# Kernel optimization log

Hardware: AMD Instinct MI355X
Metric: run time of the kernel (lower is better)

Reference implementation:

```python
import jax, jax.numpy as jnp
import numpy as np

B, T, I, H, O = 128, 2048, 128, 256, 128


def _lstm_step(h, c, x_t, wx, bx, wh, bh):
    # gates: [B, 4H], chunk order: input, forget, cell, output
    gates = x_t @ wx.T + bx + h @ wh.T + bh
    i_g, f_g, g_g, o_g = jnp.split(gates, 4, axis=1)
    i_t = jax.nn.sigmoid(i_g)
    f_t = jax.nn.sigmoid(f_g)
    g_t = jnp.tanh(g_g)
    o_t = jax.nn.sigmoid(o_g)
    cy = c * f_t + i_t * g_t
    hy = o_t * jnp.tanh(cy)
    return hy, cy


def _gru_step(h, x_t, wx, bx, wh, bh):
    # chunk order: reset, update, new
    x_g = x_t @ wx.T + bx
    h_g = h @ wh.T + bh
    x_r, x_z, x_n = jnp.split(x_g, 3, axis=1)
    h_r, h_z, h_n = jnp.split(h_g, 3, axis=1)
    r = jax.nn.sigmoid(x_r + h_r)
    z = jax.nn.sigmoid(x_z + h_z)
    n = jnp.tanh(x_n + r * h_n)
    return z * h + (1.0 - z) * n


def _run_direction(x_tbi, w1x, b1x, w1h, b1h, w2x, b2x, w2h, b2h):
    # x_tbi: [T, B, I]; returns final hidden of top cell [B, H]
    h1 = jnp.zeros((x_tbi.shape[1], H), x_tbi.dtype)
    c1 = jnp.zeros_like(h1)
    h2 = jnp.zeros_like(h1)

    def step(carry, x_t):
        h1, c1, h2 = carry
        h1, c1 = _lstm_step(h1, c1, x_t, w1x, b1x, w1h, b1h)
        h2 = _gru_step(h2, h1, w2x, b2x, w2h, b2h)
        return (h1, c1, h2), None

    (h1, c1, h2), _ = jax.lax.scan(step, (h1, c1, h2), x_tbi)
    return h2


def setup_inputs() -> dict:
    key = jax.random.key(0)
    ks = jax.random.split(key, 8)
    std1 = 1.0 / np.sqrt(H)
    u = lambda k, shape, s: jax.random.uniform(k, shape, jnp.float32, -s, s)
    x = jax.random.normal(ks[0], (B, T, I), jnp.float32)
    # Cell 1: LSTM(input=I, hidden=H)
    w1x = u(ks[1], (4 * H, I), std1)
    b1x = jnp.zeros((4 * H,), jnp.float32)
    w1h = u(ks[2], (4 * H, H), std1)
    b1h = jnp.zeros((4 * H,), jnp.float32)
    # Cell 2: GRU(input=H, hidden=H)
    w2x = u(ks[3], (3 * H, H), std1)
    b2x = jnp.zeros((3 * H,), jnp.float32)
    w2h = u(ks[4], (3 * H, H), std1)
    b2h = jnp.zeros((3 * H,), jnp.float32)
    # out_fc: Linear(2H -> O), kaiming-normal fan_in
    wo = jax.random.normal(ks[5], (O, 2 * H), jnp.float32) * np.sqrt(2.0 / (2 * H))
    bo = jnp.zeros((O,), jnp.float32)
    return {"x": x, "w1x": w1x, "b1x": b1x, "w1h": w1h, "b1h": b1h,
            "w2x": w2x, "b2x": b2x, "w2h": w2h, "b2h": b2h, "wo": wo, "bo": bo}


def reference(x, w1x, b1x, w1h, b1h, w2x, b2x, w2h, b2h, wo, bo):
    x_tbi = jnp.swapaxes(x, 0, 1)  # [T, B, I]
    h_fwd = _run_direction(x_tbi, w1x, b1x, w1h, b1h, w2x, b2x, w2h, b2h)
    h_bwd = _run_direction(x_tbi[::-1], w1x, b1x, w1h, b1h, w2x, b2x, w2h, b2h)
    h_cat = jnp.concatenate([h_fwd, h_bwd], axis=1)  # [B, 2H]
    return h_cat @ wo.T + bo  # [B, O]
```

## Files before the change

### kernel.cpp

```cpp
#include <hip/hip_runtime.h>

#define T_LEN 2048
#define I_DIM 128
#define H_DIM 256


#define XHI_OFF 0
#define XLO_OFF 8192
#define CRED_OFF 16384
#define LDS_BYTES 98304

typedef __attribute__((ext_vector_type(8))) short short8;
typedef __attribute__((ext_vector_type(16))) float f32x16;

__device__ __forceinline__ float sigmoidf_(float v) { return 1.f / (1.f + __expf(-v)); }
__device__ __forceinline__ float tanhf_fast(float v) {
    float t = __expf(-2.f * fabsf(v));
    float r = (1.f - t) / (1.f + t);
    return v < 0.f ? -r : r;
}
__device__ __forceinline__ unsigned short bf16_rne(float f) {
    unsigned u = __float_as_uint(f);
    return (unsigned short)((u + 0x7fffu + ((u >> 16) & 1u)) >> 16);
}
__device__ __forceinline__ void split2(float a, unsigned short& h, unsigned short& l) {
    h = bf16_rne(a);
    float hf = __uint_as_float(((unsigned)h) << 16);
    l = bf16_rne(a - hf);
}
__device__ __forceinline__ short8 ld_frag(const char* p) {
    union { unsigned long long u[2]; short8 s; } v;
    v.u[0] = __hip_atomic_load((const unsigned long long*)p,
                               __ATOMIC_RELAXED, __HIP_MEMORY_SCOPE_AGENT);
    v.u[1] = __hip_atomic_load((const unsigned long long*)(p + 8),
                               __ATOMIC_RELAXED, __HIP_MEMORY_SCOPE_AGENT);
    return v.s;
}

__device__ __forceinline__ void stage_unit(const float* __restrict__ x, char* smem_b,
                                           int b0, int teff, int b, int cq) {
    const float4* src = (const float4*)(x + ((size_t)(b0 + b) * T_LEN + teff) * I_DIM + cq * 16);
    float4 v0 = src[0], v1 = src[1], v2 = src[2], v3 = src[3];
    float f[16] = {v0.x, v0.y, v0.z, v0.w, v1.x, v1.y, v1.z, v1.w,
                   v2.x, v2.y, v2.z, v2.w, v3.x, v3.y, v3.z, v3.w};
    short8 H0, H1, L0, L1;
    #pragma unroll
    for (int e = 0; e < 8; ++e) {
        unsigned short h, l;
        split2(f[e], h, l);      H0[e] = (short)h; L0[e] = (short)l;
        split2(f[8 + e], h, l);  H1[e] = (short)h; L1[e] = (short)l;
    }
    char* bh = smem_b + XHI_OFF + cq * 1024 + b * 16;
    char* bl = smem_b + XLO_OFF + cq * 1024 + b * 16;
    *(short8*)bh = H0; *(short8*)(bh + 512) = H1;
    *(short8*)bl = L0; *(short8*)(bl + 512) = L1;
}

#define MFMA3(ac, ah, al, bh, bl)                                              \
    ac = __builtin_amdgcn_mfma_f32_32x32x16_bf16(ah, bh, ac, 0, 0, 0);         \
    ac = __builtin_amdgcn_mfma_f32_32x32x16_bf16(ah, bl, ac, 0, 0, 0);         \
    ac = __builtin_amdgcn_mfma_f32_32x32x16_bf16(al, bh, ac, 0, 0, 0);

#define ACCSEL(i) ((i & 3) == 0 ? acc0 : (i & 3) == 1 ? acc1 : (i & 3) == 2 ? acc2 : acc3)

__global__ __launch_bounds__(256, 1)
void brnn_persistent(const float* __restrict__ x,
                     const float* __restrict__ w1x, const float* __restrict__ b1x,
                     const float* __restrict__ w1h, const float* __restrict__ b1h,
                     const float* __restrict__ w2x, const float* __restrict__ b2x,
                     const float* __restrict__ w2h, const float* __restrict__ b2h,
                     int* flags, char* exgb, float* h2out)
{
    extern __shared__ char smem_b[];

    const int tid  = threadIdx.x;
    const int lane = tid & 63;
    const int wid  = tid >> 6;
    const int wg   = blockIdx.x;
    const int grp  = wg & 7;
    const int cu   = wg >> 3;
    const int dir  = grp >> 2;
    const int btile = grp & 3;
    const int b0   = btile * 32;

    int* flg = flags + grp * 64;
    float* cred = (float*)(smem_b + CRED_OFF);

    const int nrow = lane & 31;
    const int jrow = nrow >> 2;
    const int q    = nrow & 3;
    const int half = lane >> 5;

    short8 BH[16], BL[16];
    #pragma unroll
    for (int i = 0; i < 16; ++i) {
        short8 H, L;
        #pragma unroll
        for (int e = 0; e < 8; ++e) {
            int kk = (i & 7) * 16 + half * 8 + e;
            float v = 0.f;
            if (wid == 0) {
                if (i < 8) {
                    int R = q * H_DIM + cu * 8 + jrow;
                    v = w1x[R * I_DIM + kk];
                }
            } else if (wid == 1) {
                int R = q * H_DIM + cu * 8 + jrow;
                if (i < 8) v = w1h[R * H_DIM + kk];
                else if (q < 3) v = w2x[(q * H_DIM + cu * 8 + jrow) * H_DIM + kk];
            } else if (wid == 2) {
                int R = q * H_DIM + cu * 8 + jrow;
                if (i < 8) v = w1h[R * H_DIM + 128 + kk];
                else if (q < 3) v = w2x[(q * H_DIM + cu * 8 + jrow) * H_DIM + 128 + kk];
            } else {
                int kk16 = i * 16 + half * 8 + e;
                if (q == 0)      v = w2h[(0 * H_DIM + cu * 8 + jrow) * H_DIM + kk16];
                else if (q == 1) v = w2h[(1 * H_DIM + cu * 8 + jrow) * H_DIM + kk16];
                else if (q == 3) v = w2h[(2 * H_DIM + cu * 8 + jrow) * H_DIM + kk16];
            }
            unsigned short hh, ll;
            split2(v, hh, ll);
            H[e] = (short)hh; L[e] = (short)ll;
        }
        BH[i] = H; BL[i] = L;
    }

    const int tt  = tid & 127;
    const int bbn = tt & 31;
    const int qn  = tt >> 5;
    float biasA[2][4];
    #pragma unroll
    for (int e = 0; e < 2; ++e) {
        int jg = cu * 8 + 2 * qn + e;
        if (tid < 128) {
            #pragma unroll
            for (int g = 0; g < 4; ++g)
                biasA[e][g] = b1x[g * H_DIM + jg] + b1h[g * H_DIM + jg];
        } else {
            biasA[e][0] = b2x[0 * H_DIM + jg] + b2h[0 * H_DIM + jg];
            biasA[e][1] = b2x[1 * H_DIM + jg] + b2h[1 * H_DIM + jg];
            biasA[e][2] = b2x[2 * H_DIM + jg];
            biasA[e][3] = b2h[2 * H_DIM + jg];
        }
    }
    float st[2] = {0.f, 0.f};

    if (tid < 128) {
        char* p1 = exgb + (size_t)(8 + grp) * 65536 + (tid >> 6) * 32768
                 + (cu >> 1) * 1024 + (cu & 1) * 512 + (tid & 63) * 8;
        __hip_atomic_store((unsigned long long*)p1, 0ull,
                           __ATOMIC_RELAXED, __HIP_MEMORY_SCOPE_AGENT);
    }
    stage_unit(x, smem_b, b0, dir ? (T_LEN - 1) : 0, tid >> 3, tid & 7);
    __syncthreads();
    if (tid == 0)
        __hip_atomic_store(&flg[cu], 4, __ATOMIC_RELAXED, __HIP_MEMORY_SCOPE_AGENT);

    for (int s = 0; s <= T_LEN; ++s) {
        {
            int tgt = 4 * (s + 1);
            const int* fp = &flg[lane & 31];
            while (true) {
                int v = (lane < 32)
                    ? __hip_atomic_load(fp, __ATOMIC_RELAXED, __HIP_MEMORY_SCOPE_AGENT)
                    : 0x7fffffff;
                if (__all(v >= tgt)) break;
            }
        }
        const char* exR = exgb + (size_t)(((s + 1) & 1) * 8 + grp) * 65536;
        char*       exW = exgb + (size_t)(((s)     & 1) * 8 + grp) * 65536;

        f32x16 acc0, acc1, acc2, acc3;
        #pragma unroll
        for (int r = 0; r < 16; ++r) { acc0[r]=0.f; acc1[r]=0.f; acc2[r]=0.f; acc3[r]=0.f; }

        if (wid == 0) {
            if (s < T_LEN) {
                #pragma unroll
                for (int i = 0; i < 8; ++i) {
                    short8 ah = *(const short8*)(smem_b + XHI_OFF + i * 1024 + lane * 16);
                    short8 al = *(const short8*)(smem_b + XLO_OFF + i * 1024 + lane * 16);
                    f32x16& ac = ACCSEL(i);
                    MFMA3(ac, ah, al, BH[i], BL[i]);
                }
                float* c0 = cred;
                #pragma unroll
                for (int r = 0; r < 16; ++r) {
                    int b = (r & 3) + 8 * (r >> 2) + 4 * half;
                    c0[nrow * 33 + b] = acc0[r] + acc1[r] + acc2[r] + acc3[r];
                }
            }
        } else if (wid < 3) {
            const int sb = (wid == 1) ? 0 : 8;
            short8 hA[8], lA[8];
            #pragma unroll
            for (int i = 0; i < 8; ++i) {
                hA[i] = ld_frag(exR + (sb + i) * 1024 + lane * 16);
                lA[i] = ld_frag(exR + 32768 + (sb + i) * 1024 + lane * 16);
            }
            if (s < T_LEN) {
                #pragma unroll
                for (int i = 0; i < 8; ++i) {
                    f32x16& ac = (i & 1) ? acc1 : acc0;
                    MFMA3(ac, hA[i], lA[i], BH[i], BL[i]);
                }
            }
            if (s >= 1) {
                #pragma unroll
                for (int i = 0; i < 8; ++i) {
                    f32x16& ac = (i & 1) ? acc3 : acc2;
                    MFMA3(ac, hA[i], lA[i], BH[8 + i], BL[8 + i]);
                }
            }
            float* cL = cred + wid * 1056;
            float* cX = cred + (2 + wid) * 1056;
            #pragma unroll
            for (int r = 0; r < 16; ++r) {
                int b = (r & 3) + 8 * (r >> 2) + 4 * half;
                cL[nrow * 33 + b] = acc0[r] + acc1[r];
                cX[nrow * 33 + b] = acc2[r] + acc3[r];
            }
        } else {
            if (s >= 1) {
                short8 hA[16], lA[16];
                #pragma unroll
                for (int i = 0; i < 16; ++i) {
                    hA[i] = ld_frag(exR + (16 + i) * 1024 + lane * 16);
                    lA[i] = ld_frag(exR + 32768 + (16 + i) * 1024 + lane * 16);
                }
                #pragma unroll
                for (int i = 0; i < 16; ++i) {
                    f32x16& ac = ACCSEL(i);
                    MFMA3(ac, hA[i], lA[i], BH[i], BL[i]);
                }
                float* c5 = cred + 5 * 1056;
                #pragma unroll
                for (int r = 0; r < 16; ++r) {
                    int b = (r & 3) + 8 * (r >> 2) + 4 * half;
                    c5[nrow * 33 + b] = acc0[r] + acc1[r] + acc2[r] + acc3[r];
                }
            }
        }
        __syncthreads();

        if (tid < 128) {
            if (s < T_LEN) {
                unsigned hi32 = 0, lo32 = 0;
                #pragma unroll
                for (int e = 0; e < 2; ++e) {
                    int j = 2 * qn + e;
                    float gi = cred[(j*4+0)*33+bbn] + cred[1056+(j*4+0)*33+bbn] + cred[2112+(j*4+0)*33+bbn] + biasA[e][0];
                    float gf = cred[(j*4+1)*33+bbn] + cred[1056+(j*4+1)*33+bbn] + cred[2112+(j*4+1)*33+bbn] + biasA[e][1];
                    float gg = cred[(j*4+2)*33+bbn] + cred[1056+(j*4+2)*33+bbn] + cred[2112+(j*4+2)*33+bbn] + biasA[e][2];
                    float go = cred[(j*4+3)*33+bbn] + cred[1056+(j*4+3)*33+bbn] + cred[2112+(j*4+3)*33+bbn] + biasA[e][3];
                    float ig = sigmoidf_(gi), fg = sigmoidf_(gf);
                    float cg = tanhf_fast(gg), og = sigmoidf_(go);
                    st[e] = st[e] * fg + ig * cg;
                    float h1v = og * tanhf_fast(st[e]);
                    unsigned short h, l;
                    split2(h1v, h, l);
                    hi32 |= ((unsigned)h) << (16 * e);
                    lo32 |= ((unsigned)l) << (16 * e);
                }
                int off = (cu >> 1) * 1024 + (cu & 1) * 512 + bbn * 16 + qn * 4;
                __hip_atomic_store((unsigned*)(exW + off), hi32,
                                   __ATOMIC_RELAXED, __HIP_MEMORY_SCOPE_AGENT);
                __hip_atomic_store((unsigned*)(exW + 32768 + off), lo32,
                                   __ATOMIC_RELAXED, __HIP_MEMORY_SCOPE_AGENT);
            }
        } else {
            if (s >= 1) {
                #pragma unroll
                for (int e = 0; e < 2; ++e) {
                    int j = 2 * qn + e;
                    float rc = cred[3*1056+(j*4+0)*33+bbn] + cred[4*1056+(j*4+0)*33+bbn]
                             + cred[5*1056+(j*4+0)*33+bbn] + biasA[e][0];
                    float zc = cred[3*1056+(j*4+1)*33+bbn] + cred[4*1056+(j*4+1)*33+bbn]
                             + cred[5*1056+(j*4+1)*33+bbn] + biasA[e][1];
                    float xn = cred[3*1056+(j*4+2)*33+bbn] + cred[4*1056+(j*4+2)*33+bbn] + biasA[e][2];
                    float hn = cred[5*1056+(j*4+3)*33+bbn] + biasA[e][3];
                    float rg = sigmoidf_(rc), zg = sigmoidf_(zc);
                    float ng = tanhf_fast(xn + rg * hn);
                    st[e] = zg * st[e] + (1.f - zg) * ng;
                }
            }
            if (s == T_LEN) {
                #pragma unroll
                for (int e = 0; e < 2; ++e)
                    h2out[(size_t)(grp * 32 + bbn) * H_DIM + cu * 8 + 2 * qn + e] = st[e];
            } else {
                unsigned hi32 = 0, lo32 = 0;
                #pragma unroll
                for (int e = 0; e < 2; ++e) {
                    unsigned short h, l;
                    split2(st[e], h, l);
                    hi32 |= ((unsigned)h) << (16 * e);
                    lo32 |= ((unsigned)l) << (16 * e);
                }
                int off = 16384 + (cu >> 1) * 1024 + (cu & 1) * 512 + bbn * 16 + qn * 4;
                __hip_atomic_store((unsigned*)(exW + off), hi32,
                                   __ATOMIC_RELAXED, __HIP_MEMORY_SCOPE_AGENT);
                __hip_atomic_store((unsigned*)(exW + 32768 + off), lo32,
                                   __ATOMIC_RELAXED, __HIP_MEMORY_SCOPE_AGENT);
            }
        }

        if (s == T_LEN) break;

        asm volatile("s_waitcnt vmcnt(0)" ::: "memory");
        if (lane == 0)
            __hip_atomic_fetch_add(&flg[cu], 1, __ATOMIC_RELAXED, __HIP_MEMORY_SCOPE_AGENT);
        if (wid == 0 && s + 1 < T_LEN) {
            int teff = dir ? (T_LEN - 2 - s) : (s + 1);
            #pragma unroll
            for (int i = 0; i < 4; ++i) {
                int u = i * 64 + lane;
                stage_unit(x, smem_b, b0, teff, u >> 3, u & 7);
            }
        }
    }
}

__global__ __launch_bounds__(128)
void brnn_out(const float* __restrict__ h2out, const float* __restrict__ wo,
              const float* __restrict__ bo, float* __restrict__ out)
{
    __shared__ float hc[512];
    int b = blockIdx.x;
    int o = threadIdx.x;
    int btile = b >> 5, bi = b & 31;
    for (int k = threadIdx.x; k < 256; k += 128) {
        hc[k]       = h2out[((size_t)(btile)     * 32 + bi) * H_DIM + k];
        hc[256 + k] = h2out[((size_t)(4 + btile) * 32 + bi) * H_DIM + k];
    }
    __syncthreads();
    float acc = bo[o];
    const float4* w4 = (const float4*)&wo[(size_t)o * 512];
    #pragma unroll 8
    for (int k = 0; k < 128; ++k) {
        float4 w = w4[k];
        acc += w.x * hc[k * 4] + w.y * hc[k * 4 + 1] + w.z * hc[k * 4 + 2] + w.w * hc[k * 4 + 3];
    }
    out[b * 128 + o] = acc;
}

extern "C" void kernel_launch(void* const* d_in, const int* in_sizes, int n_in,
                              void* d_out, int out_size, void* d_ws, size_t ws_size,
                              hipStream_t stream) {
    const float* x   = (const float*)d_in[0];
    const float* w1x = (const float*)d_in[1];
    const float* b1x = (const float*)d_in[2];
    const float* w1h = (const float*)d_in[3];
    const float* b1h = (const float*)d_in[4];
    const float* w2x = (const float*)d_in[5];
    const float* b2x = (const float*)d_in[6];
    const float* w2h = (const float*)d_in[7];
    const float* b2h = (const float*)d_in[8];
    const float* wo  = (const float*)d_in[9];
    const float* bo  = (const float*)d_in[10];
    float* out = (float*)d_out;

    char* ws = (char*)d_ws;
    int* flags = (int*)ws;
    char* exgb = ws + 4096;
    float* h2out = (float*)(ws + 4096 + 1048576);

    hipMemsetAsync(flags, 0, 8 * 64 * sizeof(int), stream);

    size_t shmem = LDS_BYTES;
    hipFuncSetAttribute((const void*)brnn_persistent,
                        hipFuncAttributeMaxDynamicSharedMemorySize, (int)shmem);

    void* args[] = { (void*)&x, (void*)&w1x, (void*)&b1x, (void*)&w1h, (void*)&b1h,
                     (void*)&w2x, (void*)&b2x, (void*)&w2h, (void*)&b2h,
                     (void*)&flags, (void*)&exgb, (void*)&h2out };
    hipError_t err = hipLaunchCooperativeKernel((void*)brnn_persistent,
                                                dim3(256), dim3(256), args,
                                                (unsigned int)shmem, stream);
    if (err != hipSuccess) {
        brnn_persistent<<<dim3(256), dim3(256), shmem, stream>>>(
            x, w1x, b1x, w1h, b1h, w2x, b2x, w2h, b2h, flags, exgb, h2out);
    }

    brnn_out<<<dim3(128), dim3(128), 0, stream>>>(h2out, wo, bo, out);
}
```

Before: 13.76 ms.

## Interleave forward and backward directions within each workgroup, halving grid size

Each workgroup now processes both the forward and backward direction for one batch tile, alternating phases so one direction's flag wait can overlap the other's compute. The grid shrinks from 256 to 128 workgroups, and LDS holds separate x staging buffers and reduction scratch for each direction. Per-step synchronisation changes from per-wave atomic increments to a block-wide __syncthreads followed by a single store of the step counter. The intent is to hide the cross-workgroup sync latency of the serial recurrence behind the other direction's work. The cost is twice the serial work per workgroup and an added block barrier on every phase.

```diff
diff --git a/kernel.cpp b/kernel.cpp
--- a/kernel.cpp
+++ b/kernel.cpp
@@ -5,9 +5,9 @@
 #define H_DIM 256
 
 
-#define XHI_OFF 0
-#define XLO_OFF 8192
-#define CRED_OFF 16384
+#define XA_OFF 0
+#define XB_OFF 16384
+#define CRED_OFF 32768
 #define LDS_BYTES 98304
 
 typedef __attribute__((ext_vector_type(8))) short short8;
@@ -37,7 +37,7 @@
     return v.s;
 }
 
-__device__ __forceinline__ void stage_unit(const float* __restrict__ x, char* smem_b,
+__device__ __forceinline__ void stage_unit(const float* __restrict__ x, char* xbuf,
                                            int b0, int teff, int b, int cq) {
     const float4* src = (const float4*)(x + ((size_t)(b0 + b) * T_LEN + teff) * I_DIM + cq * 16);
     float4 v0 = src[0], v1 = src[1], v2 = src[2], v3 = src[3];
@@ -50,8 +50,8 @@
         split2(f[e], h, l);      H0[e] = (short)h; L0[e] = (short)l;
         split2(f[8 + e], h, l);  H1[e] = (short)h; L1[e] = (short)l;
     }
-    char* bh = smem_b + XHI_OFF + cq * 1024 + b * 16;
-    char* bl = smem_b + XLO_OFF + cq * 1024 + b * 16;
+    char* bh = xbuf + cq * 1024 + b * 16;
+    char* bl = xbuf + 8192 + cq * 1024 + b * 16;
     *(short8*)bh = H0; *(short8*)(bh + 512) = H1;
     *(short8*)bl = L0; *(short8*)(bl + 512) = L1;
 }
@@ -77,14 +77,18 @@
     const int lane = tid & 63;
     const int wid  = tid >> 6;
     const int wg   = blockIdx.x;
-    const int grp  = wg & 7;
-    const int cu   = wg >> 3;
-    const int dir  = grp >> 2;
-    const int btile = grp & 3;
+    const int btile = wg & 3;
+    const int cu   = wg >> 2;
+    const int grpA = btile;
+    const int grpB = 4 + btile;
     const int b0   = btile * 32;
 
-    int* flg = flags + grp * 64;
-    float* cred = (float*)(smem_b + CRED_OFF);
+    int* flgA = flags + grpA * 64;
+    int* flgB = flags + grpB * 64;
+    float* credA = (float*)(smem_b + CRED_OFF);
+    float* credB = credA + 6 * 1056;
+    char* xbufA = smem_b + XA_OFF;
+    char* xbufB = smem_b + XB_OFF;
 
     const int nrow = lane & 31;
     const int jrow = nrow >> 2;
@@ -143,22 +147,31 @@
             biasA[e][3] = b2h[2 * H_DIM + jg];
         }
     }
-    float st[2] = {0.f, 0.f};
-
-    if (tid < 128) {
-        char* p1 = exgb + (size_t)(8 + grp) * 65536 + (tid >> 6) * 32768
+    float stA[2] = {0.f, 0.f};
+    float stB[2] = {0.f, 0.f};
+
+    {
+        int plane = (tid & 127) >> 6;
+        int g = (tid < 128) ? grpA : grpB;
+        char* p1 = exgb + (size_t)(8 + g) * 65536 + plane * 32768
                  + (cu >> 1) * 1024 + (cu & 1) * 512 + (tid & 63) * 8;
         __hip_atomic_store((unsigned long long*)p1, 0ull,
                            __ATOMIC_RELAXED, __HIP_MEMORY_SCOPE_AGENT);
     }
-    stage_unit(x, smem_b, b0, dir ? (T_LEN - 1) : 0, tid >> 3, tid & 7);
+    stage_unit(x, xbufA, b0, 0, tid >> 3, tid & 7);
+    stage_unit(x, xbufB, b0, T_LEN - 1, tid >> 3, tid & 7);
     __syncthreads();
-    if (tid == 0)
-        __hip_atomic_store(&flg[cu], 4, __ATOMIC_RELAXED, __HIP_MEMORY_SCOPE_AGENT);
-
-    for (int s = 0; s <= T_LEN; ++s) {
+    if (tid == 0) {
+        __hip_atomic_store(&flgA[cu], 1, __ATOMIC_RELAXED, __HIP_MEMORY_SCOPE_AGENT);
+        __hip_atomic_store(&flgB[cu], 1, __ATOMIC_RELAXED, __HIP_MEMORY_SCOPE_AGENT);
+    }
+
+    auto phase = [&](int grp, int dir, char* xbuf, float* cred6, int* flg,
+                     float (&st2)[2], int s) {
+        const char* exR = exgb + (size_t)(((s + 1) & 1) * 8 + grp) * 65536;
+        char*       exW = exgb + (size_t)(((s)     & 1) * 8 + grp) * 65536;
         {
-            int tgt = 4 * (s + 1);
+            int tgt = s + 1;
             const int* fp = &flg[lane & 31];
             while (true) {
                 int v = (lane < 32)
@@ -167,9 +180,6 @@
                 if (__all(v >= tgt)) break;
             }
         }
-        const char* exR = exgb + (size_t)(((s + 1) & 1) * 8 + grp) * 65536;
-        char*       exW = exgb + (size_t)(((s)     & 1) * 8 + grp) * 65536;
-
         f32x16 acc0, acc1, acc2, acc3;
         #pragma unroll
         for (int r = 0; r < 16; ++r) { acc0[r]=0.f; acc1[r]=0.f; acc2[r]=0.f; acc3[r]=0.f; }
@@ -178,12 +188,12 @@
             if (s < T_LEN) {
                 #pragma unroll
                 for (int i = 0; i < 8; ++i) {
-                    short8 ah = *(const short8*)(smem_b + XHI_OFF + i * 1024 + lane * 16);
-                    short8 al = *(const short8*)(smem_b + XLO_OFF + i * 1024 + lane * 16);
+                    short8 ah = *(const short8*)(xbuf + i * 1024 + lane * 16);
+                    short8 al = *(const short8*)(xbuf + 8192 + i * 1024 + lane * 16);
                     f32x16& ac = ACCSEL(i);
                     MFMA3(ac, ah, al, BH[i], BL[i]);
                 }
-                float* c0 = cred;
+                float* c0 = cred6;
                 #pragma unroll
                 for (int r = 0; r < 16; ++r) {
                     int b = (r & 3) + 8 * (r >> 2) + 4 * half;
@@ -212,8 +222,8 @@
                     MFMA3(ac, hA[i], lA[i], BH[8 + i], BL[8 + i]);
                 }
             }
-            float* cL = cred + wid * 1056;
-            float* cX = cred + (2 + wid) * 1056;
+            float* cL = cred6 + wid * 1056;
+            float* cX = cred6 + (2 + wid) * 1056;
             #pragma unroll
             for (int r = 0; r < 16; ++r) {
                 int b = (r & 3) + 8 * (r >> 2) + 4 * half;
@@ -233,7 +243,7 @@
                     f32x16& ac = ACCSEL(i);
                     MFMA3(ac, hA[i], lA[i], BH[i], BL[i]);
                 }
-                float* c5 = cred + 5 * 1056;
+                float* c5 = cred6 + 5 * 1056;
                 #pragma unroll
                 for (int r = 0; r < 16; ++r) {
                     int b = (r & 3) + 8 * (r >> 2) + 4 * half;
@@ -249,14 +259,14 @@
                 #pragma unroll
                 for (int e = 0; e < 2; ++e) {
                     int j = 2 * qn + e;
-                    float gi = cred[(j*4+0)*33+bbn] + cred[1056+(j*4+0)*33+bbn] + cred[2112+(j*4+0)*33+bbn] + biasA[e][0];
-                    float gf = cred[(j*4+1)*33+bbn] + cred[1056+(j*4+1)*33+bbn] + cred[2112+(j*4+1)*33+bbn] + biasA[e][1];
-                    float gg = cred[(j*4+2)*33+bbn] + cred[1056+(j*4+2)*33+bbn] + cred[2112+(j*4+2)*33+bbn] + biasA[e][2];
-                    float go = cred[(j*4+3)*33+bbn] + cred[1056+(j*4+3)*33+bbn] + cred[2112+(j*4+3)*33+bbn] + biasA[e][3];
+                    float gi = cred6[(j*4+0)*33+bbn] + cred6[1056+(j*4+0)*33+bbn] + cred6[2112+(j*4+0)*33+bbn] + biasA[e][0];
+                    float gf = cred6[(j*4+1)*33+bbn] + cred6[1056+(j*4+1)*33+bbn] + cred6[2112+(j*4+1)*33+bbn] + biasA[e][1];
+                    float gg = cred6[(j*4+2)*33+bbn] + cred6[1056+(j*4+2)*33+bbn] + cred6[2112+(j*4+2)*33+bbn] + biasA[e][2];
+                    float go = cred6[(j*4+3)*33+bbn] + cred6[1056+(j*4+3)*33+bbn] + cred6[2112+(j*4+3)*33+bbn] + biasA[e][3];
                     float ig = sigmoidf_(gi), fg = sigmoidf_(gf);
                     float cg = tanhf_fast(gg), og = sigmoidf_(go);
-                    st[e] = st[e] * fg + ig * cg;
-                    float h1v = og * tanhf_fast(st[e]);
+                    st2[e] = st2[e] * fg + ig * cg;
+                    float h1v = og * tanhf_fast(st2[e]);
                     unsigned short h, l;
                     split2(h1v, h, l);
                     hi32 |= ((unsigned)h) << (16 * e);
@@ -273,27 +283,27 @@
                 #pragma unroll
                 for (int e = 0; e < 2; ++e) {
                     int j = 2 * qn + e;
-                    float rc = cred[3*1056+(j*4+0)*33+bbn] + cred[4*1056+(j*4+0)*33+bbn]
-                             + cred[5*1056+(j*4+0)*33+bbn] + biasA[e][0];
-                    float zc = cred[3*1056+(j*4+1)*33+bbn] + cred[4*1056+(j*4+1)*33+bbn]
-                             + cred[5*1056+(j*4+1)*33+bbn] + biasA[e][1];
-                    float xn = cred[3*1056+(j*4+2)*33+bbn] + cred[4*1056+(j*4+2)*33+bbn] + biasA[e][2];
-                    float hn = cred[5*1056+(j*4+3)*33+bbn] + biasA[e][3];
+                    float rc = cred6[3*1056+(j*4+0)*33+bbn] + cred6[4*1056+(j*4+0)*33+bbn]
+                             + cred6[5*1056+(j*4+0)*33+bbn] + biasA[e][0];
+                    float zc = cred6[3*1056+(j*4+1)*33+bbn] + cred6[4*1056+(j*4+1)*33+bbn]
+                             + cred6[5*1056+(j*4+1)*33+bbn] + biasA[e][1];
+                    float xn = cred6[3*1056+(j*4+2)*33+bbn] + cred6[4*1056+(j*4+2)*33+bbn] + biasA[e][2];
+                    float hn = cred6[5*1056+(j*4+3)*33+bbn] + biasA[e][3];
                     float rg = sigmoidf_(rc), zg = sigmoidf_(zc);
                     float ng = tanhf_fast(xn + rg * hn);
-                    st[e] = zg * st[e] + (1.f - zg) * ng;
+                    st2[e] = zg * st2[e] + (1.f - zg) * ng;
                 }
             }
             if (s == T_LEN) {
                 #pragma unroll
                 for (int e = 0; e < 2; ++e)
-                    h2out[(size_t)(grp * 32 + bbn) * H_DIM + cu * 8 + 2 * qn + e] = st[e];
+                    h2out[(size_t)(grp * 32 + bbn) * H_DIM + cu * 8 + 2 * qn + e] = st2[e];
             } else {
                 unsigned hi32 = 0, lo32 = 0;
                 #pragma unroll
                 for (int e = 0; e < 2; ++e) {
                     unsigned short h, l;
-                    split2(st[e], h, l);
+                    split2(st2[e], h, l);
                     hi32 |= ((unsigned)h) << (16 * e);
                     lo32 |= ((unsigned)l) << (16 * e);
                 }
@@ -305,19 +315,22 @@
             }
         }
 
-        if (s == T_LEN) break;
-
-        asm volatile("s_waitcnt vmcnt(0)" ::: "memory");
-        if (lane == 0)
-            __hip_atomic_fetch_add(&flg[cu], 1, __ATOMIC_RELAXED, __HIP_MEMORY_SCOPE_AGENT);
+        __syncthreads();
+        if (tid == 0 && s < T_LEN)
+            __hip_atomic_store(&flg[cu], s + 2, __ATOMIC_RELAXED, __HIP_MEMORY_SCOPE_AGENT);
         if (wid == 0 && s + 1 < T_LEN) {
             int teff = dir ? (T_LEN - 2 - s) : (s + 1);
             #pragma unroll
             for (int i = 0; i < 4; ++i) {
                 int u = i * 64 + lane;
-                stage_unit(x, smem_b, b0, teff, u >> 3, u & 7);
-            }
-        }
+                stage_unit(x, xbuf, b0, teff, u >> 3, u & 7);
+            }
+        }
+    };
+
+    for (int s = 0; s <= T_LEN; ++s) {
+        phase(grpA, 0, xbufA, credA, flgA, stA, s);
+        phase(grpB, 1, xbufB, credB, flgB, stB, s);
     }
 }
 
@@ -375,10 +388,10 @@
                      (void*)&w2x, (void*)&b2x, (void*)&w2h, (void*)&b2h,
                      (void*)&flags, (void*)&exgb, (void*)&h2out };
     hipError_t err = hipLaunchCooperativeKernel((void*)brnn_persistent,
-                                                dim3(256), dim3(256), args,
+                                                dim3(128), dim3(256), args,
                                                 (unsigned int)shmem, stream);
     if (err != hipSuccess) {
-        brnn_persistent<<<dim3(256), dim3(256), shmem, stream>>>(
+        brnn_persistent<<<dim3(128), dim3(256), shmem, stream>>>(
             x, w1x, b1x, w1h, b1h, w2x, b2x, w2h, b2h, flags, exgb, h2out);
     }
 
```

Result: slower. 20.68 ms (+50.3%).
